# Optimization experiments

Measured on AMD Instinct MI355X. Metric: run time of the kernel, lower is better.

## Reference

```python
import jax, jax.numpy as jnp
import numpy as np

C1, C2, C3, S = 3, 6, 3, 16
SPLITS = (9 * C1 * 1, C1, 9 * C2 * C1, C2, 9 * C3 * C2, C3, 9 * S * C3, S)  # sums to 811
B = 16384


def _channelize(w, cin, cout):
    # w: [B, cout*9*cin] -> filter [3, 3, cin, B*cout] (B-major on out axis)
    w = w.reshape(-1, cout, 9 * cin)
    w = jnp.transpose(w, (2, 0, 1))          # [9*cin, B, cout]
    return w.reshape(3, 3, cin, -1)


def _gconv(x, w, groups):
    # x: [1, H, W, B*cin], w: [3, 3, cin, B*cout]; grouped conv, groups=B
    return jax.lax.conv_general_dilated(
        x, w, window_strides=(1, 1), padding='VALID',
        dimension_numbers=('NHWC', 'HWIO', 'NHWC'),
        feature_group_count=groups)


def _maxpool2(x):
    return jax.lax.reduce_window(x, -jnp.inf, jax.lax.max,
                                 (1, 2, 2, 1), (1, 2, 2, 1), 'VALID')


def setup_inputs() -> dict:
    key = jax.random.key(0)
    ks = jax.random.split(key, 8)
    tot = sum(SPLITS)
    return {
        'image': jax.random.normal(ks[0], (1, 28, 28, B), jnp.float32),
        'state': jax.random.normal(ks[1], (B, S), jnp.float32),
        'W1': jax.random.normal(ks[2], (S, 16), jnp.float32) * 0.25,
        'b1': jnp.zeros((16,), jnp.float32),
        'W2': jax.random.normal(ks[3], (16, 16), jnp.float32) * 0.25,
        'b2': jnp.zeros((16,), jnp.float32),
        'W3': jax.random.normal(ks[4], (16, tot), jnp.float32) * 0.1,
        'b3': jnp.zeros((tot,), jnp.float32),
    }


def reference(image, state, W1, b1, W2, b2, W3, b3):
    batch = state.shape[0]
    # Hypernetwork MLP producing per-sample conv weights (dropout rate 0 => identity)
    h = jax.nn.relu(state @ W1 + b1)
    h = jax.nn.relu(h @ W2 + b2)
    w = h @ W3 + b3                               # [B, 811]
    idx = np.cumsum(SPLITS)[:-1]
    w1, bb1, w2, bb2, w3, bb3, w4, bb4 = jnp.split(w, idx, axis=1)

    x = _gconv(image, _channelize(w1, 1, C1), batch) + bb1.reshape(-1)   # [1,26,26,B*C1]
    x = _maxpool2(jax.nn.relu(x))                                        # [1,13,13,B*C1]
    x = _gconv(x, _channelize(w2, C1, C2), batch) + bb2.reshape(-1)      # [1,11,11,B*C2]
    x = _maxpool2(jax.nn.relu(x))                                        # [1,5,5,B*C2]
    x = _gconv(x, _channelize(w3, C2, C3), batch) + bb3.reshape(-1)      # [1,3,3,B*C3]
    x = jax.nn.relu(x)
    x = _gconv(x, _channelize(w4, C3, S), batch) + bb4.reshape(-1)       # [1,1,1,B*S]
    x = jnp.transpose(x, (3, 1, 2, 0)).reshape(-1, S)                    # [B, S]
    return state + x
```

## Files before the change

### kernel.cpp

```cpp
#include <hip/hip_runtime.h>

#define BLK   256
#define NSAMP 4
#define REG   1072
#define OFF_P2   0
#define OFF_P3   152
#define HWW      784
#define HW_P1    1596
#define DW_P1    798


__device__ __forceinline__ float bf2f(unsigned short u) {
    return __uint_as_float(((unsigned int)u) << 16);
}
__device__ __forceinline__ unsigned short f2bf(float f) {
    unsigned int x = __float_as_uint(f);
    return (unsigned short)((x + 0x7fffu + ((x >> 16) & 1u)) >> 16);
}
__device__ __forceinline__ void wsync() {
    __builtin_amdgcn_wave_barrier();
    __asm__ volatile("s_waitcnt lgkmcnt(0)" ::: "memory");
    __builtin_amdgcn_wave_barrier();
}

__device__ __forceinline__ bool is_bf16(const void* p, int elems) {
    const unsigned short* h = (const unsigned short*)p;
    int n = elems; if (n > 32) n = 32;
    int nz = 0, ok = 0;
    for (int i = 0; i < n; i += 2) {
        unsigned short u = h[i];
        if (u == 0) continue;
        ++nz;
        unsigned int e = (u >> 7) & 255u;
        if (e >= 100u && e <= 141u) ++ok;
    }
    if (nz < 4) return true;
    return 4 * ok >= 3 * nz;
}

__global__ __launch_bounds__(BLK, 5)
void dyncnn4_kernel(const void* __restrict__ image,
                    const void* __restrict__ state,
                    const void* __restrict__ W1, const void* __restrict__ b1,
                    const void* __restrict__ W2, const void* __restrict__ b2,
                    const void* __restrict__ W3, const void* __restrict__ b3,
                    void* __restrict__ out,
                    int B, int nswz)
{
    __shared__ float SH[NSAMP * REG];
    __shared__ float s_st[NSAMP][16];
    __shared__ float s_h1[NSAMP][16];
    __shared__ float s_h2[NSAMP][16];

    const int t    = threadIdx.x;
    const int wv   = t >> 6;
    const int lane = t & 63;

    const bool im_bf = is_bf16(image, 784 * B);
    const bool st_bf = is_bf16(state, 16 * B);
    const bool w1_bf = is_bf16(W1, 256);
    const bool b1_bf = is_bf16(b1, 16);
    const bool w2_bf = is_bf16(W2, 256);
    const bool b2_bf = is_bf16(b2, 16);
    const bool w3_bf = is_bf16(W3, 12976);
    const bool b3_bf = is_bf16(b3, 811);
    const bool out_bf = im_bf && st_bf && w1_bf && w2_bf && w3_bf;

    int p = blockIdx.x;
    int l = (nswz > 0) ? ((p & 7) * nswz + (p >> 3)) : p;
    const int b0 = l * NSAMP;

    unsigned short* su = (unsigned short*)SH;

    if (wv == 0) {
        int s = lane >> 4, j = lane & 15;
        int gi = (b0 + s) * 16 + j;
        s_st[s][j] = st_bf ? bf2f(((const unsigned short*)state)[gi])
                           : ((const float*)state)[gi];
        wsync();
        float acc = b1_bf ? bf2f(((const unsigned short*)b1)[j])
                          : ((const float*)b1)[j];
#pragma unroll
        for (int k = 0; k < 16; ++k) {
            float w = w1_bf ? bf2f(((const unsigned short*)W1)[k * 16 + j])
                            : ((const float*)W1)[k * 16 + j];
            acc += s_st[s][k] * w;
        }
        s_h1[s][j] = fmaxf(acc, 0.f);
        wsync();
        acc = b2_bf ? bf2f(((const unsigned short*)b2)[j])
                    : ((const float*)b2)[j];
#pragma unroll
        for (int k = 0; k < 16; ++k) {
            float w = w2_bf ? bf2f(((const unsigned short*)W2)[k * 16 + j])
                            : ((const float*)W2)[k * 16 + j];
            acc += s_h1[s][k] * w;
        }
        s_h2[s][j] = fmaxf(acc, 0.f);
    } else {
        if (im_bf) {
            const unsigned short* im = (const unsigned short*)image;
            for (int pix = t - 64; pix < 784; pix += 192) {
                const uint2 v = *(const uint2*)(im + pix * B + b0);
                su[0 * 2 * REG + pix] = (unsigned short)(v.x);
                su[1 * 2 * REG + pix] = (unsigned short)(v.x >> 16);
                su[2 * 2 * REG + pix] = (unsigned short)(v.y);
                su[3 * 2 * REG + pix] = (unsigned short)(v.y >> 16);
            }
        } else {
            const float* im = (const float*)image;
            for (int pix = t - 64; pix < 784; pix += 192) {
                const float4 v = *(const float4*)(im + pix * B + b0);
                su[0 * 2 * REG + pix] = f2bf(v.x);
                su[1 * 2 * REG + pix] = f2bf(v.y);
                su[2 * 2 * REG + pix] = f2bf(v.z);
                su[3 * 2 * REG + pix] = f2bf(v.w);
            }
        }
    }
    __syncthreads();

    {
        float h2r[4][16];
        const float4* hp = (const float4*)&s_h2[0][0];
#pragma unroll
        for (int i = 0; i < 16; ++i) {
            float4 v = hp[i];
            h2r[i >> 2][(i & 3) * 4 + 0] = v.x;
            h2r[i >> 2][(i & 3) * 4 + 1] = v.y;
            h2r[i >> 2][(i & 3) * 4 + 2] = v.z;
            h2r[i >> 2][(i & 3) * 4 + 3] = v.w;
        }
        for (int j = t; j < 811; j += BLK) {
            float bb = b3_bf ? bf2f(((const unsigned short*)b3)[j])
                             : ((const float*)b3)[j];
            float a0 = bb, a1 = bb, a2 = bb, a3 = bb;
            if (w3_bf) {
                const unsigned short* q = (const unsigned short*)W3 + j;
#pragma unroll
                for (int k = 0; k < 16; ++k) {
                    float w = bf2f(q[k * 811]);
                    a0 += h2r[0][k] * w; a1 += h2r[1][k] * w;
                    a2 += h2r[2][k] * w; a3 += h2r[3][k] * w;
                }
            } else {
                const float* q = (const float*)W3 + j;
#pragma unroll
                for (int k = 0; k < 16; ++k) {
                    float w = q[k * 811];
                    a0 += h2r[0][k] * w; a1 += h2r[1][k] * w;
                    a2 += h2r[2][k] * w; a3 += h2r[3][k] * w;
                }
            }
            su[0 * 2 * REG + HWW + j] = f2bf(a0);
            su[1 * 2 * REG + HWW + j] = f2bf(a1);
            su[2 * 2 * REG + HWW + j] = f2bf(a2);
            su[3 * 2 * REG + HWW + j] = f2bf(a3);
        }
    }
    __syncthreads();

    const int sb  = wv * REG;
    const int sb2 = wv * 2 * REG;

    {
        float wc[27], cb[3];
#pragma unroll
        for (int i = 0; i < 27; ++i) wc[i] = bf2f(su[sb2 + HWW + i]);
#pragma unroll
        for (int c = 0; c < 3; ++c) cb[c] = bf2f(su[sb2 + HWW + 27 + c]);
        const unsigned* suw = (const unsigned*)&SH[sb];
#pragma unroll
        for (int it = 0; it < 3; ++it) {
            int pix = lane + it * 64;
            if (pix < 169) {
                int py = pix / 13, px = pix - py * 13;
                int iy = 2 * py;
                float pt[4][4];
#pragma unroll
                for (int dy = 0; dy < 4; ++dy) {
                    int r = (iy + dy) * 14 + px;
                    unsigned d0 = suw[r], d1 = suw[r + 1];
                    pt[dy][0] = __uint_as_float(d0 << 16);
                    pt[dy][1] = __uint_as_float(d0 & 0xffff0000u);
                    pt[dy][2] = __uint_as_float(d1 << 16);
                    pt[dy][3] = __uint_as_float(d1 & 0xffff0000u);
                }
                unsigned short* op = &su[sb2 + HW_P1 + py * 14 + px];
#pragma unroll
                for (int c = 0; c < 3; ++c) {
                    float a00 = 0.f, a01 = 0.f, a10 = 0.f, a11 = 0.f;
#pragma unroll
                    for (int ky = 0; ky < 3; ++ky)
#pragma unroll
                        for (int kx = 0; kx < 3; ++kx) {
                            float w = wc[c * 9 + ky * 3 + kx];
                            a00 += pt[ky][kx] * w;
                            a01 += pt[ky][kx + 1] * w;
                            a10 += pt[ky + 1][kx] * w;
                            a11 += pt[ky + 1][kx + 1] * w;
                        }
                    float m = fmaxf(fmaxf(a00, a01), fmaxf(a10, a11));
                    op[c * 182] = f2bf(fmaxf(m + cb[c], 0.f));
                }
            }
        }
    }
    wsync();

    {
        int g = lane >> 5, q = lane & 31;
        if (q < 25) {
            int py = q / 5, px = q - py * 5;
            const unsigned* p1w = (const unsigned*)&SH[sb + DW_P1];
            float acc[3][4];
#pragma unroll
            for (int it = 0; it < 3; ++it)
#pragma unroll
                for (int i = 0; i < 4; ++i) acc[it][i] = 0.f;
#pragma unroll
            for (int ci = 0; ci < 3; ++ci) {
                float pt[4][4];
#pragma unroll
                for (int dy = 0; dy < 4; ++dy) {
                    int r = ci * 91 + (2 * py + dy) * 7 + px;
                    unsigned d0 = p1w[r], d1 = p1w[r + 1];
                    pt[dy][0] = __uint_as_float(d0 << 16);
                    pt[dy][1] = __uint_as_float(d0 & 0xffff0000u);
                    pt[dy][2] = __uint_as_float(d1 << 16);
                    pt[dy][3] = __uint_as_float(d1 & 0xffff0000u);
                }
#pragma unroll
                for (int it = 0; it < 3; ++it) {
                    int c = it * 2 + g;
                    const int wo = sb2 + HWW + 30 + c * 27 + ci;
#pragma unroll
                    for (int ky = 0; ky < 3; ++ky)
#pragma unroll
                        for (int kx = 0; kx < 3; ++kx) {
                            float w = bf2f(su[wo + (ky * 3 + kx) * 3]);
                            acc[it][0] += pt[ky][kx] * w;
                            acc[it][1] += pt[ky][kx + 1] * w;
                            acc[it][2] += pt[ky + 1][kx] * w;
                            acc[it][3] += pt[ky + 1][kx + 1] * w;
                        }
                }
            }
#pragma unroll
            for (int it = 0; it < 3; ++it) {
                int c = it * 2 + g;
                float m = fmaxf(fmaxf(acc[it][0], acc[it][1]),
                                fmaxf(acc[it][2], acc[it][3]));
                SH[sb + OFF_P2 + c * 25 + q] =
                    fmaxf(m + bf2f(su[sb2 + HWW + 192 + c]), 0.f);
            }
        }
    }
    wsync();

    {
        float acc = 0.f;
        int pq = lane % 27;
        int half = lane / 27;
        int c = pq / 9, pos = pq - c * 9;
        int py = pos / 3, px = pos - py * 3;
        if (lane < 54) {
            const int wo = sb2 + HWW + 198 + c * 54;
            const int cb3 = half * 3;
#pragma unroll
            for (int ky = 0; ky < 3; ++ky)
#pragma unroll
                for (int kx = 0; kx < 3; ++kx)
#pragma unroll
                    for (int ci = 0; ci < 3; ++ci)
                        acc += SH[sb + OFF_P2 + (cb3 + ci) * 25 + (py + ky) * 5 + px + kx] *
                               bf2f(su[wo + (ky * 3 + kx) * 6 + cb3 + ci]);
        }
        float other = __shfl(acc, (lane + 27) & 63);
        if (lane < 27)
            SH[sb + OFF_P3 + pq] =
                fmaxf(acc + other + bf2f(su[sb2 + HWW + 360 + c]), 0.f);
    }
    wsync();

    {
        float acc = 0.f;
        int os = lane & 15, h = (lane >> 4) & 1;
        if (lane < 32) {
            const int wo = sb2 + HWW + 363 + os * 27;
            int p0 = h ? 4 : 0, p1 = h ? 9 : 4;
            for (int pp = p0; pp < p1; ++pp)
#pragma unroll
                for (int ci = 0; ci < 3; ++ci)
                    acc += SH[sb + OFF_P3 + ci * 9 + pp] *
                           bf2f(su[wo + pp * 3 + ci]);
        }
        float other = __shfl(acc, (lane + 16) & 63);
        if (lane < 16) {
            float tot = acc + other + bf2f(su[sb2 + HWW + 795 + os]) + s_st[wv][os];
            int gi = (b0 + wv) * 16 + os;
            if (out_bf) ((unsigned short*)out)[gi] = f2bf(tot);
            else        ((float*)out)[gi] = tot;
        }
    }
}

extern "C" void kernel_launch(void* const* d_in, const int* in_sizes, int n_in,
                              void* d_out, int out_size, void* d_ws, size_t ws_size,
                              hipStream_t stream) {
    (void)d_ws; (void)ws_size; (void)n_in; (void)out_size;
    int B = in_sizes[1] / 16;
    int nblocks = B / NSAMP;
    int nswz = (nblocks % 8 == 0) ? (nblocks / 8) : 0;

    dyncnn4_kernel<<<nblocks, BLK, 0, stream>>>(
        d_in[0], d_in[1], d_in[2], d_in[3], d_in[4], d_in[5], d_in[6], d_in[7],
        d_out, B, nswz);
}
```

Before: 163.3 us.

## Process eight samples per 512-thread block and parallelize dtype detection

New measurement: 162.3 us. About the same (-0.6%).

```diff
diff --git a/kernel.cpp b/kernel.cpp
--- a/kernel.cpp
+++ b/kernel.cpp
@@ -1,7 +1,7 @@
 #include <hip/hip_runtime.h>
 
-#define BLK   256
-#define NSAMP 4
+#define BLK   512
+#define NSAMP 8
 #define REG   1072
 #define OFF_P2   0
 #define OFF_P3   152
@@ -38,7 +38,7 @@
     return 4 * ok >= 3 * nz;
 }
 
-__global__ __launch_bounds__(BLK, 5)
+__global__ __launch_bounds__(BLK, 4)
 void dyncnn4_kernel(const void* __restrict__ image,
                     const void* __restrict__ state,
                     const void* __restrict__ W1, const void* __restrict__ b1,
@@ -51,19 +51,29 @@
     __shared__ float s_st[NSAMP][16];
     __shared__ float s_h1[NSAMP][16];
     __shared__ float s_h2[NSAMP][16];
+    __shared__ unsigned char s_fl[8];
 
     const int t    = threadIdx.x;
     const int wv   = t >> 6;
     const int lane = t & 63;
 
-    const bool im_bf = is_bf16(image, 784 * B);
-    const bool st_bf = is_bf16(state, 16 * B);
-    const bool w1_bf = is_bf16(W1, 256);
-    const bool b1_bf = is_bf16(b1, 16);
-    const bool w2_bf = is_bf16(W2, 256);
-    const bool b2_bf = is_bf16(b2, 16);
-    const bool w3_bf = is_bf16(W3, 12976);
-    const bool b3_bf = is_bf16(b3, 811);
+    if (t < 8) {
+        const void* q; int n;
+        switch (t) {
+            case 0:  q = image; n = 784 * B; break;
+            case 1:  q = state; n = 16 * B;  break;
+            case 2:  q = W1;    n = 256;     break;
+            case 3:  q = b1;    n = 16;      break;
+            case 4:  q = W2;    n = 256;     break;
+            case 5:  q = b2;    n = 16;      break;
+            case 6:  q = W3;    n = 12976;   break;
+            default: q = b3;    n = 811;     break;
+        }
+        s_fl[t] = is_bf16(q, n) ? 1 : 0;
+    }
+    __syncthreads();
+    const bool im_bf = s_fl[0], st_bf = s_fl[1], w1_bf = s_fl[2], b1_bf = s_fl[3];
+    const bool w2_bf = s_fl[4], b2_bf = s_fl[5], w3_bf = s_fl[6], b3_bf = s_fl[7];
     const bool out_bf = im_bf && st_bf && w1_bf && w2_bf && w3_bf;
 
     int p = blockIdx.x;
@@ -72,8 +82,8 @@
 
     unsigned short* su = (unsigned short*)SH;
 
-    if (wv == 0) {
-        int s = lane >> 4, j = lane & 15;
+    if (wv < 2) {
+        int s = wv * 4 + (lane >> 4), j = lane & 15;
         int gi = (b0 + s) * 16 + j;
         s_st[s][j] = st_bf ? bf2f(((const unsigned short*)state)[gi])
                            : ((const float*)state)[gi];
@@ -100,62 +110,61 @@
     } else {
         if (im_bf) {
             const unsigned short* im = (const unsigned short*)image;
-            for (int pix = t - 64; pix < 784; pix += 192) {
-                const uint2 v = *(const uint2*)(im + pix * B + b0);
+            for (int pix = t - 128; pix < 784; pix += 384) {
+                const uint4 v = *(const uint4*)(im + pix * B + b0);
                 su[0 * 2 * REG + pix] = (unsigned short)(v.x);
                 su[1 * 2 * REG + pix] = (unsigned short)(v.x >> 16);
                 su[2 * 2 * REG + pix] = (unsigned short)(v.y);
                 su[3 * 2 * REG + pix] = (unsigned short)(v.y >> 16);
+                su[4 * 2 * REG + pix] = (unsigned short)(v.z);
+                su[5 * 2 * REG + pix] = (unsigned short)(v.z >> 16);
+                su[6 * 2 * REG + pix] = (unsigned short)(v.w);
+                su[7 * 2 * REG + pix] = (unsigned short)(v.w >> 16);
             }
         } else {
             const float* im = (const float*)image;
-            for (int pix = t - 64; pix < 784; pix += 192) {
-                const float4 v = *(const float4*)(im + pix * B + b0);
-                su[0 * 2 * REG + pix] = f2bf(v.x);
-                su[1 * 2 * REG + pix] = f2bf(v.y);
-                su[2 * 2 * REG + pix] = f2bf(v.z);
-                su[3 * 2 * REG + pix] = f2bf(v.w);
+            for (int pix = t - 128; pix < 784; pix += 384) {
+                const float4 a = *(const float4*)(im + pix * B + b0);
+                const float4 c = *(const float4*)(im + pix * B + b0 + 4);
+                su[0 * 2 * REG + pix] = f2bf(a.x);
+                su[1 * 2 * REG + pix] = f2bf(a.y);
+                su[2 * 2 * REG + pix] = f2bf(a.z);
+                su[3 * 2 * REG + pix] = f2bf(a.w);
+                su[4 * 2 * REG + pix] = f2bf(c.x);
+                su[5 * 2 * REG + pix] = f2bf(c.y);
+                su[6 * 2 * REG + pix] = f2bf(c.z);
+                su[7 * 2 * REG + pix] = f2bf(c.w);
             }
         }
     }
     __syncthreads();
 
-    {
-        float h2r[4][16];
-        const float4* hp = (const float4*)&s_h2[0][0];
-#pragma unroll
-        for (int i = 0; i < 16; ++i) {
-            float4 v = hp[i];
-            h2r[i >> 2][(i & 3) * 4 + 0] = v.x;
-            h2r[i >> 2][(i & 3) * 4 + 1] = v.y;
-            h2r[i >> 2][(i & 3) * 4 + 2] = v.z;
-            h2r[i >> 2][(i & 3) * 4 + 3] = v.w;
-        }
+#pragma unroll
+    for (int sp = 0; sp < NSAMP; sp += 2) {
+        float h2a[16], h2b[16];
+#pragma unroll
+        for (int k = 0; k < 16; ++k) { h2a[k] = s_h2[sp][k]; h2b[k] = s_h2[sp + 1][k]; }
         for (int j = t; j < 811; j += BLK) {
             float bb = b3_bf ? bf2f(((const unsigned short*)b3)[j])
                              : ((const float*)b3)[j];
-            float a0 = bb, a1 = bb, a2 = bb, a3 = bb;
+            float aa = bb, ab = bb;
             if (w3_bf) {
                 const unsigned short* q = (const unsigned short*)W3 + j;
 #pragma unroll
                 for (int k = 0; k < 16; ++k) {
                     float w = bf2f(q[k * 811]);
-                    a0 += h2r[0][k] * w; a1 += h2r[1][k] * w;
-                    a2 += h2r[2][k] * w; a3 += h2r[3][k] * w;
+                    aa += h2a[k] * w; ab += h2b[k] * w;
                 }
             } else {
                 const float* q = (const float*)W3 + j;
 #pragma unroll
                 for (int k = 0; k < 16; ++k) {
                     float w = q[k * 811];
-                    a0 += h2r[0][k] * w; a1 += h2r[1][k] * w;
-                    a2 += h2r[2][k] * w; a3 += h2r[3][k] * w;
-                }
-            }
-            su[0 * 2 * REG + HWW + j] = f2bf(a0);
-            su[1 * 2 * REG + HWW + j] = f2bf(a1);
-            su[2 * 2 * REG + HWW + j] = f2bf(a2);
-            su[3 * 2 * REG + HWW + j] = f2bf(a3);
+                    aa += h2a[k] * w; ab += h2b[k] * w;
+                }
+            }
+            su[sp * 2 * REG + HWW + j]       = f2bf(aa);
+            su[(sp + 1) * 2 * REG + HWW + j] = f2bf(ab);
         }
     }
     __syncthreads();
```
